# Kernel optimization log

Hardware: AMD Instinct MI355X
Metric: run time of the kernel (lower is better)

## Reference

```python
import jax, jax.numpy as jnp
import numpy as np

B, L, D = 1, 4096, 1024
H, DH = 16, 64
BASE = 10000.0


def _rope_tables(L, dh, dtype=jnp.float32):
    inv_freq = 1.0 / (BASE ** (jnp.arange(0, dh, 2, dtype=jnp.float32) / dh))
    freqs = jnp.outer(jnp.arange(L, dtype=jnp.float32), inv_freq)  # [L, dh/2]
    return jnp.cos(freqs).astype(dtype), jnp.sin(freqs).astype(dtype)


def _apply_rope(x, cos, sin):
    # x: [B,H,L,dh]; cos/sin: [L,dh/2]
    x1, x2 = x[..., ::2], x[..., 1::2]
    c = cos[None, None]
    s = sin[None, None]
    return jnp.concatenate([x1 * c - x2 * s, x1 * s + x2 * c], axis=-1)


def setup_inputs() -> dict:
    key = jax.random.key(0)
    ks = jax.random.split(key, 5)
    x = jax.random.normal(ks[0], (B, L, D), dtype=jnp.float32)
    mask = jnp.tril(jnp.ones((L, L), dtype=jnp.int32))  # causal 0/1 mask
    sd = 1.0 / np.sqrt(D)
    Wq = jax.random.normal(ks[1], (D, D), dtype=jnp.float32) * sd
    Wk = jax.random.normal(ks[2], (D, D), dtype=jnp.float32) * sd
    Wv = jax.random.normal(ks[3], (D, D), dtype=jnp.float32) * sd
    Wo = jax.random.normal(ks[4], (D, D), dtype=jnp.float32) * sd
    return {"x": x, "mask": mask, "Wq": Wq, "Wk": Wk, "Wv": Wv, "Wo": Wo}


def reference(x, mask, Wq, Wk, Wv, Wo):
    b, l, d = x.shape
    scale = DH ** -0.5
    cos, sin = _rope_tables(l, DH, x.dtype)

    def heads(w):
        return (x @ w.T).reshape(b, l, H, DH).transpose(0, 2, 1, 3)  # [B,H,L,dh]

    q = _apply_rope(heads(Wq), cos, sin)
    k = _apply_rope(heads(Wk), cos, sin)
    v = heads(Wv)

    attn = jnp.einsum('bhqd,bhkd->bhqk', q, k) * scale
    attn = jnp.where(mask[:l, :l] == 0, -jnp.inf, attn)
    attn = jax.nn.softmax(attn, axis=-1)
    out = jnp.einsum('bhqk,bhkd->bhqd', attn, v)
    out = out.transpose(0, 2, 1, 3).reshape(b, l, d)
    return out @ Wo.T
```

## Files before the change

### kernel.cpp

```cpp
#include <hip/hip_runtime.h>
#include <math.h>

#define LSEQ   4096
#define DMODEL 1024
#define NH     16
#define DHEAD  64
#define PSTRIDE 40
#define MASKV  -30000.0f
#define C2SCALE 0.18033688f

typedef __attribute__((ext_vector_type(8))) short  bf16x8;
typedef __attribute__((ext_vector_type(4))) float  floatx4;
typedef unsigned short ushort_t;

#if __has_builtin(__builtin_amdgcn_exp2f)
#define EXP2F __builtin_amdgcn_exp2f
#else
#define EXP2F exp2f
#endif

__device__ __forceinline__ ushort_t f2bf(float x) {
  unsigned u = __builtin_bit_cast(unsigned, x);
  return (ushort_t)((u + 0x7fff + ((u >> 16) & 1)) >> 16);
}
__device__ __forceinline__ unsigned bf16pair(float a, float b) {
  return (unsigned)f2bf(a) | ((unsigned)f2bf(b) << 16);
}
__device__ __forceinline__ unsigned bfpack_trunc(float a, float b) {
  return __builtin_amdgcn_perm(__builtin_bit_cast(unsigned, b),
                               __builtin_bit_cast(unsigned, a), 0x07060302u);
}
__device__ __forceinline__ void gl_lds16(const ushort_t* g, ushort_t* l) {
  __builtin_amdgcn_global_load_lds(
      (const __attribute__((address_space(1))) void*)g,
      (__attribute__((address_space(3))) void*)l, 16, 0, 0);
}

__global__ void rope_table(float2* __restrict__ rope) {
  const int idx = blockIdx.x * 256 + threadIdx.x;
  const int s = idx >> 5, t = idx & 31;
  const double invf = exp((double)t * -0.28782313662425572);
  const double ang = (double)s * invf;
  rope[idx] = make_float2((float)cos(ang), (float)sin(ang));
}

__global__ void cvt_bf16(const float* __restrict__ x,  const float* __restrict__ wq,
                         const float* __restrict__ wk, const float* __restrict__ wv,
                         const float* __restrict__ wo, ushort_t* __restrict__ dst) {
  const size_t e = ((size_t)blockIdx.x * 256 + threadIdx.x) * 4;
  const float* src; size_t off;
  if      (e < (size_t)(4u << 20)) { src = x;  off = e; }
  else if (e < (size_t)(5u << 20)) { src = wq; off = e - (size_t)(4u << 20); }
  else if (e < (size_t)(6u << 20)) { src = wk; off = e - (size_t)(5u << 20); }
  else if (e < (size_t)(7u << 20)) { src = wv; off = e - (size_t)(6u << 20); }
  else                             { src = wo; off = e - (size_t)(7u << 20); }
  const float4 v = *(const float4*)(src + off);
  uint2 p; p.x = bf16pair(v.x, v.y); p.y = bf16pair(v.z, v.w);
  *(uint2*)(dst + e) = p;
}

template<int MODE>
__global__ __launch_bounds__(256)
void mfma_gemm(const ushort_t* __restrict__ A, const ushort_t* __restrict__ B,
               float* __restrict__ C, const float2* __restrict__ rope,
               ushort_t* __restrict__ Qo, ushort_t* __restrict__ Ko,
               ushort_t* __restrict__ Vo) {
  __shared__ ushort_t As[128 * 64];
  __shared__ ushort_t Bs[128 * 64];
  const int tid  = threadIdx.x;
  const int w    = tid >> 6, lane = tid & 63;
  const int wm   = w >> 1,   wn   = w & 1;
  const int quad = lane >> 4, col = lane & 15;
  const int csw  = col & 7;
  const int i0 = blockIdx.x * 128;
  const int j0 = blockIdx.y * 128;

  const ushort_t* Ab = A + (size_t)i0 * DMODEL;
  const ushort_t* Bb = B + (size_t)j0 * DMODEL;

  floatx4 acc[4][4];
#pragma unroll
  for (int mt = 0; mt < 4; ++mt)
#pragma unroll
    for (int nt = 0; nt < 4; ++nt) acc[mt][nt] = (floatx4){0.f, 0.f, 0.f, 0.f};

  const int lrow = lane >> 3;
  const int lcol = ((lane & 7) ^ lrow) * 8;

  for (int k0 = 0; k0 < DMODEL; k0 += 64) {
    __syncthreads();
#pragma unroll
    for (int it = 0; it < 4; ++it) {
      const int rb = (it * 4 + w) * 8;
      gl_lds16(Ab + (size_t)(rb + lrow) * DMODEL + k0 + lcol, As + rb * 64);
      gl_lds16(Bb + (size_t)(rb + lrow) * DMODEL + k0 + lcol, Bs + rb * 64);
    }
    __syncthreads();

#pragma unroll
    for (int kk = 0; kk < 64; kk += 32) {
      const int cblk = (kk >> 3) + quad;
      bf16x8 af[4], bfr[4];
#pragma unroll
      for (int mt = 0; mt < 4; ++mt)
        af[mt] = *(const bf16x8*)(As + (wm * 64 + mt * 16 + col) * 64 +
                                  ((cblk ^ csw) * 8));
#pragma unroll
      for (int nt = 0; nt < 4; ++nt)
        bfr[nt] = *(const bf16x8*)(Bs + (wn * 64 + nt * 16 + col) * 64 +
                                   ((cblk ^ csw) * 8));
#pragma unroll
      for (int mt = 0; mt < 4; ++mt)
#pragma unroll
        for (int nt = 0; nt < 4; ++nt)
          acc[mt][nt] = __builtin_amdgcn_mfma_f32_16x16x32_bf16(
              af[mt], bfr[nt], acc[mt][nt], 0, 0, 0);
    }
  }

  if (MODE == 0) {
#pragma unroll
    for (int mt = 0; mt < 4; ++mt) {
      const int i = i0 + wm * 64 + mt * 16 + quad * 4;
#pragma unroll
      for (int nt = 0; nt < 4; ++nt) {
        const int j = j0 + wn * 64 + nt * 16 + col;
#pragma unroll
        for (int r = 0; r < 4; ++r)
          C[(size_t)(i + r) * DMODEL + j] = acc[mt][nt][r];
      }
    }
  } else {
    const int which = i0 >> 10;
#pragma unroll
    for (int mt = 0; mt < 4; ++mt) {
      const int f0 = i0 + wm * 64 + mt * 16 + quad * 4;
      const int h  = (f0 >> 6) & 15;
      const int d  = f0 & 63;
      if (which == 2) {
#pragma unroll
        for (int nt = 0; nt < 4; ++nt) {
          const int s = j0 + wn * 64 + nt * 16 + col;
#pragma unroll
          for (int r = 0; r < 4; ++r)
            Vo[(size_t)(h * DHEAD + d + r) * LSEQ + s] = f2bf(acc[mt][nt][r]);
        }
      } else {
        ushort_t* dst = which ? Ko : Qo;
        const float qs = which ? 1.0f : C2SCALE;
        const int t0 = d >> 1;
#pragma unroll
        for (int nt = 0; nt < 4; ++nt) {
          const int s = j0 + wn * 64 + nt * 16 + col;
          const float4 cst = *(const float4*)((const float*)rope + ((size_t)s << 6) + t0 * 2);
          ushort_t* ob = dst + ((size_t)h * LSEQ + s) * DHEAD;
          const float x1 = acc[mt][nt][0], x2 = acc[mt][nt][1];
          const float y1 = acc[mt][nt][2], y2 = acc[mt][nt][3];
          *(unsigned*)(ob + t0)      = bf16pair((x1 * cst.x - x2 * cst.y) * qs,
                                                (y1 * cst.z - y2 * cst.w) * qs);
          *(unsigned*)(ob + t0 + 32) = bf16pair((x1 * cst.y + x2 * cst.x) * qs,
                                                (y1 * cst.w + y2 * cst.z) * qs);
        }
      }
    }
  }
}

__global__ __launch_bounds__(1024, 4)
void attn_mfma(const ushort_t* __restrict__ Qh, const ushort_t* __restrict__ Kh,
               const ushort_t* __restrict__ Vt, ushort_t* __restrict__ Om) {
  const int h   = blockIdx.x;
  const int g   = blockIdx.y;
  const int tid = threadIdx.x;
  const int w     = tid >> 6;
  const int wl    = w & 3;
  const int half  = (w >> 2) & 1;
  const int ktpar = w >> 3;
  const int wg    = w & 7;
  const int lane = tid & 63;
  const int quad = lane >> 4;
  const int col  = lane & 15;
  const int csw  = col & 7;

  __shared__ __align__(16) char smem[106496];
  ushort_t* Ks   = (ushort_t*)smem;
  ushort_t* Vs   = (ushort_t*)(smem + 32768);
  ushort_t* Ps   = (ushort_t*)(smem + 65536);
  float*    Obuf = (float*)smem;
  __shared__ float lbuf[3][4][2][16];
  ushort_t* psw = Ps + w * (32 * PSTRIDE);

  const int srow = wg * 8 + (lane >> 3);
  const int scol = (((lane & 7) ^ ((lane >> 3) & 7)) * 8);

  for (int pass = 0; pass < 2; ++pass) {
    const int qb      = pass ? (31 - g) : g;
    const int qbase   = qb * 128 + wl * 32;
    const int nkt_max = 2 * qb + 2;
    const int nt2     = nkt_max >> 1;

    bf16x8 qf[2][2];
#pragma unroll
    for (int nq = 0; nq < 2; ++nq)
#pragma unroll
      for (int c = 0; c < 2; ++c)
        qf[nq][c] = *(const bf16x8*)(Qh +
            ((size_t)(h * LSEQ + qbase + nq * 16 + col)) * DHEAD + quad * 8 + c * 32);

    floatx4 ot[4][2];
#pragma unroll
    for (int md = 0; md < 4; ++md)
#pragma unroll
      for (int nq = 0; nq < 2; ++nq) ot[md][nq] = (floatx4){0.f, 0.f, 0.f, 0.f};
    float l_[2] = {0.f, 0.f};

    auto stage = [&](int kt, int b) {
      const int key0 = kt * 64;
      const int boff = (ktpar * 2 + b) * 4096;
      gl_lds16(Kh + ((size_t)(h * LSEQ + key0 + srow)) * DHEAD + scol,
               Ks + boff + wg * 512);
      gl_lds16(Vt + ((size_t)(h * DHEAD + srow)) * LSEQ + key0 + scol,
               Vs + boff + wg * 512);
    };

    stage(ktpar, 0);
    __syncthreads();

    for (int ktt = 0; ktt < nt2; ++ktt) {
      const int kt  = 2 * ktt + ktpar;
      const int buf = ktt & 1;
      if (ktt + 1 < nt2) stage(kt + 2, buf ^ 1);

      const ushort_t* kb = Ks + (ktpar * 2 + buf) * 4096;
      const ushort_t* vb = Vs + (ktpar * 2 + buf) * 4096;

      bf16x8 kf[2][2];
#pragma unroll
      for (int mk = 0; mk < 2; ++mk)
#pragma unroll
        for (int c = 0; c < 2; ++c)
          kf[mk][c] = *(const bf16x8*)(kb + (half * 32 + mk * 16 + col) * 64 +
                                       (((c * 4 + quad) ^ csw) * 8));

      floatx4 st[2][2];
#pragma unroll
      for (int mk = 0; mk < 2; ++mk)
#pragma unroll
        for (int nq = 0; nq < 2; ++nq) st[mk][nq] = (floatx4){0.f, 0.f, 0.f, 0.f};
#pragma unroll
      for (int mk = 0; mk < 2; ++mk)
#pragma unroll
        for (int c = 0; c < 2; ++c)
#pragma unroll
          for (int nq = 0; nq < 2; ++nq)
            st[mk][nq] = __builtin_amdgcn_mfma_f32_16x16x32_bf16(
                kf[mk][c], qf[nq][c], st[mk][nq], 0, 0, 0);

      if (kt >= nkt_max - 2) {
        const int key0 = kt * 64 + half * 32;
#pragma unroll
        for (int mk = 0; mk < 2; ++mk) {
          const int keyb = key0 + mk * 16 + quad * 4;
#pragma unroll
          for (int nq = 0; nq < 2; ++nq) {
            const int q = qbase + nq * 16 + col;
#pragma unroll
            for (int r = 0; r < 4; ++r)
              if (keyb + r > q) st[mk][nq][r] = MASKV;
          }
        }
      }

#pragma unroll
      for (int mk = 0; mk < 2; ++mk)
#pragma unroll
        for (int nq = 0; nq < 2; ++nq) {
#pragma unroll
          for (int r = 0; r < 4; ++r) st[mk][nq][r] = EXP2F(st[mk][nq][r]);
          l_[nq] += (st[mk][nq][0] + st[mk][nq][1]) + (st[mk][nq][2] + st[mk][nq][3]);
        }

#pragma unroll
      for (int mk = 0; mk < 2; ++mk)
#pragma unroll
        for (int nq = 0; nq < 2; ++nq) {
          uint2 pk;
          pk.x = bfpack_trunc(st[mk][nq][0], st[mk][nq][1]);
          pk.y = bfpack_trunc(st[mk][nq][2], st[mk][nq][3]);
          *(uint2*)(psw + (nq * 16 + col) * PSTRIDE + mk * 16 + quad * 4) = pk;
        }
      bf16x8 pf[2];
#pragma unroll
      for (int nq = 0; nq < 2; ++nq)
        pf[nq] = *(const bf16x8*)(psw + (nq * 16 + col) * PSTRIDE + quad * 8);

      bf16x8 vf[4];
#pragma unroll
      for (int md = 0; md < 4; ++md)
        vf[md] = *(const bf16x8*)(vb + (md * 16 + col) * 64 +
                                  (((half * 4 + quad) ^ csw) * 8));
#pragma unroll
      for (int md = 0; md < 4; ++md)
#pragma unroll
        for (int nq = 0; nq < 2; ++nq)
          ot[md][nq] = __builtin_amdgcn_mfma_f32_16x16x32_bf16(
              vf[md], pf[nq], ot[md][nq], 0, 0, 0);

      __syncthreads();
    }

    float lr[2];
#pragma unroll
    for (int nq = 0; nq < 2; ++nq) {
      float ls = l_[nq];
      ls += __shfl_xor(ls, 16);
      ls += __shfl_xor(ls, 32);
      lr[nq] = ls;
    }

    const int di = ((half << 1) | ktpar) - 1;
    if (di >= 0) {
#pragma unroll
      for (int nq = 0; nq < 2; ++nq) {
        if (quad == 0) lbuf[di][wl][nq][col] = lr[nq];
#pragma unroll
        for (int md = 0; md < 4; ++md)
          *(float4*)(Obuf + di * 8704 + ((wl * 2 + nq) * 16 + col) * 68 + md * 16 + quad * 4) =
              (float4){ot[md][nq][0], ot[md][nq][1], ot[md][nq][2], ot[md][nq][3]};
      }
    }
    __syncthreads();

    if (di < 0) {
#pragma unroll
      for (int nq = 0; nq < 2; ++nq) {
        const float inv = 1.0f / (lr[nq] + lbuf[0][wl][nq][col] +
                                  lbuf[1][wl][nq][col] + lbuf[2][wl][nq][col]);
        const int q = qbase + nq * 16 + col;
#pragma unroll
        for (int md = 0; md < 4; ++md) {
          const int ob_off = ((wl * 2 + nq) * 16 + col) * 68 + md * 16 + quad * 4;
          const float4 o0 = *(const float4*)(Obuf + ob_off);
          const float4 o1 = *(const float4*)(Obuf + 8704 + ob_off);
          const float4 o2 = *(const float4*)(Obuf + 17408 + ob_off);
          uint2 pk;
          pk.x = bf16pair((ot[md][nq][0] + o0.x + o1.x + o2.x) * inv,
                          (ot[md][nq][1] + o0.y + o1.y + o2.y) * inv);
          pk.y = bf16pair((ot[md][nq][2] + o0.z + o1.z + o2.z) * inv,
                          (ot[md][nq][3] + o0.w + o1.w + o2.w) * inv);
          *(uint2*)(Om + (size_t)q * DMODEL + h * DHEAD + md * 16 + quad * 4) = pk;
        }
      }
    }
    __syncthreads();
  }
}

extern "C" void kernel_launch(void* const* d_in, const int* in_sizes, int n_in,
                              void* d_out, int out_size, void* d_ws, size_t ws_size,
                              hipStream_t stream) {
  const float* x  = (const float*)d_in[0];
  const float* Wq = (const float*)d_in[2];
  const float* Wk = (const float*)d_in[3];
  const float* Wv = (const float*)d_in[4];
  const float* Wo = (const float*)d_in[5];
  float* out = (float*)d_out;

  const size_t M1 = (size_t)1 << 20;
  ushort_t* xb  = (ushort_t*)d_ws;
  ushort_t* Wb  = xb  + 4 * M1;
  ushort_t* wob = Wb  + 3 * M1;
  ushort_t* Qh  = wob + 1 * M1;
  ushort_t* Kh  = Qh  + 4 * M1;
  ushort_t* Vt  = Kh  + 4 * M1;
  ushort_t* Om  = Vt  + 4 * M1;
  float2*   rope = (float2*)(Om + 4 * M1);

  rope_table<<<512, 256, 0, stream>>>(rope);
  cvt_bf16<<<8192, 256, 0, stream>>>(x, Wq, Wk, Wv, Wo, xb);
  mfma_gemm<1><<<dim3(3072 / 128, LSEQ / 128), 256, 0, stream>>>(
      Wb, xb, nullptr, rope, Qh, Kh, Vt);
  attn_mfma<<<dim3(NH, 16), 1024, 0, stream>>>(Qh, Kh, Vt, Om);
  mfma_gemm<0><<<dim3(LSEQ / 128, DMODEL / 128), 256, 0, stream>>>(
      Om, wob, out, nullptr, nullptr, nullptr, nullptr);
}
```

Baseline: 246.5 us.

## Replace QKV projection GEMM with 256x256-tile, 512-thread pipelined kernel

Adds a dedicated QKV projection kernel that computes 256x256 output tiles with 8 waves, double-buffered direct global-to-LDS loads, and split-phase prefetch interleaved with MFMA groups under raised wave priority. The fused RoPE, scaling and V-transpose epilogue is kept. Larger tiles raise operand reuse and cut global traffic per FLOP. In exchange the grid shrinks to 192 blocks on a 256-CU device, and the kernel needs 128 KB of LDS plus many accumulator registers, which may limit occupancy.

```diff
diff --git a/kernel.cpp b/kernel.cpp
--- a/kernel.cpp
+++ b/kernel.cpp
@@ -57,6 +57,148 @@
   const float4 v = *(const float4*)(src + off);
   uint2 p; p.x = bf16pair(v.x, v.y); p.y = bf16pair(v.z, v.w);
   *(uint2*)(dst + e) = p;
+}
+
+__global__ __launch_bounds__(512, 2)
+void gemm256_qkv(const ushort_t* __restrict__ A, const ushort_t* __restrict__ B,
+                 const float2* __restrict__ rope,
+                 ushort_t* __restrict__ Qo, ushort_t* __restrict__ Ko,
+                 ushort_t* __restrict__ Vo) {
+  __shared__ __align__(16) ushort_t smem[65536];
+  const int tid  = threadIdx.x;
+  const int w    = tid >> 6, lane = tid & 63;
+  const int wr   = w >> 2,   wc   = w & 3;
+  const int quad = lane >> 4, col = lane & 15;
+  const int csw  = col & 7;
+  const int i0 = blockIdx.x * 256;
+  const int j0 = blockIdx.y * 256;
+
+  const ushort_t* Ab = A + (size_t)i0 * DMODEL;
+  const ushort_t* Bb = B + (size_t)j0 * DMODEL;
+
+  const int sr8 = lane >> 3;
+  const int sc  = ((lane & 7) ^ sr8) * 8;
+
+  floatx4 acc[8][4];
+#pragma unroll
+  for (int m = 0; m < 8; ++m)
+#pragma unroll
+    for (int n = 0; n < 4; ++n) acc[m][n] = (floatx4){0.f, 0.f, 0.f, 0.f};
+
+  auto stageA = [&](int kt, int h) {
+    ushort_t* dst = smem + (kt & 1) * 16384 + (h * 128 + w * 8) * 64;
+    const ushort_t* src = Ab + (size_t)(h * 128 + w * 8 + sr8) * DMODEL + kt * 64 + sc;
+    gl_lds16(src, dst);
+    gl_lds16(src + (size_t)64 * DMODEL, dst + 4096);
+  };
+  auto stageB = [&](int kt, int h) {
+    ushort_t* dst = smem + 32768 + (kt & 1) * 16384 + (h * 128 + w * 8) * 64;
+    const ushort_t* src = Bb + (size_t)(h * 128 + w * 8 + sr8) * DMODEL + kt * 64 + sc;
+    gl_lds16(src, dst);
+    gl_lds16(src + (size_t)64 * DMODEL, dst + 4096);
+  };
+
+  stageA(0, 0); stageB(0, 0); stageA(0, 1); stageB(0, 1);
+  asm volatile("s_waitcnt vmcnt(0)" ::: "memory");
+  __builtin_amdgcn_s_barrier();
+
+#pragma unroll 2
+  for (int t = 0; t < 16; ++t) {
+    const ushort_t* As_ = smem + (t & 1) * 16384;
+    const ushort_t* Bs_ = smem + 32768 + (t & 1) * 16384;
+    const bool pre = (t + 1 < 16);
+
+    bf16x8 af[4], bfr[4];
+#pragma unroll
+    for (int n = 0; n < 4; ++n)
+      bfr[n] = *(const bf16x8*)(Bs_ + (wc * 64 + n * 16 + col) * 64 + ((quad ^ csw) * 8));
+#pragma unroll
+    for (int m = 0; m < 4; ++m)
+      af[m] = *(const bf16x8*)(As_ + (wr * 128 + m * 16 + col) * 64 + ((quad ^ csw) * 8));
+    if (pre) { stageA(t + 1, 0); stageB(t + 1, 0); }
+    __builtin_amdgcn_s_setprio(1);
+#pragma unroll
+    for (int m = 0; m < 4; ++m)
+#pragma unroll
+      for (int n = 0; n < 4; ++n)
+        acc[m][n] = __builtin_amdgcn_mfma_f32_16x16x32_bf16(af[m], bfr[n], acc[m][n], 0, 0, 0);
+    __builtin_amdgcn_s_setprio(0);
+    __builtin_amdgcn_s_barrier();
+
+#pragma unroll
+    for (int m = 0; m < 4; ++m)
+      af[m] = *(const bf16x8*)(As_ + (wr * 128 + (m + 4) * 16 + col) * 64 + ((quad ^ csw) * 8));
+    if (pre) { stageA(t + 1, 1); stageB(t + 1, 1); }
+    __builtin_amdgcn_s_setprio(1);
+#pragma unroll
+    for (int m = 0; m < 4; ++m)
+#pragma unroll
+      for (int n = 0; n < 4; ++n)
+        acc[m + 4][n] = __builtin_amdgcn_mfma_f32_16x16x32_bf16(af[m], bfr[n], acc[m + 4][n], 0, 0, 0);
+    __builtin_amdgcn_s_setprio(0);
+    __builtin_amdgcn_s_barrier();
+
+#pragma unroll
+    for (int n = 0; n < 4; ++n)
+      bfr[n] = *(const bf16x8*)(Bs_ + (wc * 64 + n * 16 + col) * 64 + (((4 + quad) ^ csw) * 8));
+#pragma unroll
+    for (int m = 0; m < 4; ++m)
+      af[m] = *(const bf16x8*)(As_ + (wr * 128 + m * 16 + col) * 64 + (((4 + quad) ^ csw) * 8));
+    __builtin_amdgcn_s_setprio(1);
+#pragma unroll
+    for (int m = 0; m < 4; ++m)
+#pragma unroll
+      for (int n = 0; n < 4; ++n)
+        acc[m][n] = __builtin_amdgcn_mfma_f32_16x16x32_bf16(af[m], bfr[n], acc[m][n], 0, 0, 0);
+    __builtin_amdgcn_s_setprio(0);
+    __builtin_amdgcn_s_barrier();
+
+#pragma unroll
+    for (int m = 0; m < 4; ++m)
+      af[m] = *(const bf16x8*)(As_ + (wr * 128 + (m + 4) * 16 + col) * 64 + (((4 + quad) ^ csw) * 8));
+    __builtin_amdgcn_s_setprio(1);
+#pragma unroll
+    for (int m = 0; m < 4; ++m)
+#pragma unroll
+      for (int n = 0; n < 4; ++n)
+        acc[m + 4][n] = __builtin_amdgcn_mfma_f32_16x16x32_bf16(af[m], bfr[n], acc[m + 4][n], 0, 0, 0);
+    __builtin_amdgcn_s_setprio(0);
+    asm volatile("s_waitcnt vmcnt(0)" ::: "memory");
+    __builtin_amdgcn_s_barrier();
+  }
+
+  const int which = i0 >> 10;
+#pragma unroll
+  for (int m = 0; m < 8; ++m) {
+    const int f0 = i0 + wr * 128 + m * 16 + quad * 4;
+    const int h  = (f0 >> 6) & 15;
+    const int d  = f0 & 63;
+    if (which == 2) {
+#pragma unroll
+      for (int n = 0; n < 4; ++n) {
+        const int s = j0 + wc * 64 + n * 16 + col;
+#pragma unroll
+        for (int r = 0; r < 4; ++r)
+          Vo[(size_t)(h * DHEAD + d + r) * LSEQ + s] = f2bf(acc[m][n][r]);
+      }
+    } else {
+      ushort_t* dst = which ? Ko : Qo;
+      const float qs = which ? 1.0f : C2SCALE;
+      const int t0 = d >> 1;
+#pragma unroll
+      for (int n = 0; n < 4; ++n) {
+        const int s = j0 + wc * 64 + n * 16 + col;
+        const float4 cst = *(const float4*)((const float*)rope + ((size_t)s << 6) + t0 * 2);
+        ushort_t* ob = dst + ((size_t)h * LSEQ + s) * DHEAD;
+        const float x1 = acc[m][n][0], x2 = acc[m][n][1];
+        const float y1 = acc[m][n][2], y2 = acc[m][n][3];
+        *(unsigned*)(ob + t0)      = bf16pair((x1 * cst.x - x2 * cst.y) * qs,
+                                              (y1 * cst.z - y2 * cst.w) * qs);
+        *(unsigned*)(ob + t0 + 32) = bf16pair((x1 * cst.y + x2 * cst.x) * qs,
+                                              (y1 * cst.w + y2 * cst.z) * qs);
+      }
+    }
+  }
 }
 
 template<int MODE>
@@ -378,8 +520,8 @@
 
   rope_table<<<512, 256, 0, stream>>>(rope);
   cvt_bf16<<<8192, 256, 0, stream>>>(x, Wq, Wk, Wv, Wo, xb);
-  mfma_gemm<1><<<dim3(3072 / 128, LSEQ / 128), 256, 0, stream>>>(
-      Wb, xb, nullptr, rope, Qh, Kh, Vt);
+  gemm256_qkv<<<dim3(3072 / 256, LSEQ / 256), 512, 0, stream>>>(
+      Wb, xb, rope, Qh, Kh, Vt);
   attn_mfma<<<dim3(NH, 16), 1024, 0, stream>>>(Qh, Kh, Vt, Om);
   mfma_gemm<0><<<dim3(LSEQ / 128, DMODEL / 128), 256, 0, stream>>>(
       Om, wob, out, nullptr, nullptr, nullptr, nullptr);
```

Result: faster. 239.5 us (-2.8%).
